# Optimization experiments

Measured on AMD Instinct MI355X. Metric: run time of the kernel, lower is better.

Reference implementation:

```python
import jax, jax.numpy as jnp
import numpy as np
import math

TWO_PI = 2.0 * math.pi
LN_EPS = 1e-5


def _phase(pos_f, d):
    # periods[i, j] = i * d + j + 2 ; phi[s, i, j] = cos(2*pi*k_s / periods[i, j])
    i = jnp.arange(d, dtype=jnp.float32)
    periods = i[:, None] * d + i[None, :] + 2.0  # (d, d)
    return jnp.cos(TWO_PI * pos_f[:, None, None] / periods)  # (S, d, d)


def _layernorm(x, g, b):
    mu = jnp.mean(x, axis=-1, keepdims=True)
    var = jnp.mean(jnp.square(x - mu), axis=-1, keepdims=True)
    return (x - mu) * jax.lax.rsqrt(var + LN_EPS) * g + b


def _pos_nk(x, P, phi):
    # Nk[b, s, i] = sum_j P[i, j] * x[b, s, j] * phi[s, i, j]
    return jnp.einsum('bsj,ij,sij->bsi', x, P, phi)


def setup_inputs() -> dict:
    key = jax.random.key(0)
    ks = jax.random.split(key, 10)
    B, S, V, D = 4, 4096, 64, 128
    NTOK = 64  # 4^3 k-mer tokens
    u = lambda k, shp, a: jax.random.uniform(k, shp, jnp.float32, -a, a)
    return {
        'tokens': jax.random.randint(ks[0], (B, S), 0, NTOK, dtype=jnp.int32),
        'positions': jnp.arange(S, dtype=jnp.int32),
        'emb': jax.random.normal(ks[1], (NTOK, V), jnp.float32),
        'char_P': u(ks[2], (V, V), 0.1),
        'M1': u(ks[3], (D, V), 0.5),
        'P1': u(ks[4], (D, D), 0.1),
        'g1': jnp.ones((D,), jnp.float32),
        'b1': jnp.zeros((D,), jnp.float32),
        'R1': u(ks[5], (D, V), 0.1),
        'M2': u(ks[6], (D, D), 0.5),
        'P2': u(ks[7], (D, D), 0.1),
        'g2': jnp.ones((D,), jnp.float32),
        'b2': jnp.zeros((D,), jnp.float32),
    }


def reference(tokens, positions, emb, char_P, M1, P1, g1, b1, R1, M2, P2, g2, b2):
    pos_f = positions.astype(jnp.float32)
    V, D1, D2 = emb.shape[1], M1.shape[0], M2.shape[0]
    # char level (Layer 0): embedding + position-modulated mixing
    x = emb[tokens]                               # (B, S, V)
    h = _pos_nk(x, char_P, _phase(pos_f, V))      # (B, S, V)
    # Layer 1: separate residual (in_dim != out_dim -> linear proj)
    t1 = jnp.einsum('bsj,ij->bsi', h, M1)         # (B, S, D1)
    n1 = _pos_nk(_layernorm(t1, g1, b1), P1, _phase(pos_f, D1))
    h1 = n1 + jnp.einsum('bsj,ij->bsi', h, R1)
    # Layer 2: shared residual (residual = x @ M.T, pre-norm)
    t2 = jnp.einsum('bsj,ij->bsi', h1, M2)        # (B, S, D2)
    n2 = _pos_nk(_layernorm(t2, g2, b2), P2, _phase(pos_f, D2))
    return n2 + t2
```

## Files before the change

kernel.cpp:

```cpp
#include <hip/hip_runtime.h>

typedef unsigned short u16;
typedef unsigned int   u32;
typedef float f32x2 __attribute__((ext_vector_type(2)));

#define BB 4
#define SS 4096
#define VV 64
#define DD 128

#define CPT_OFF 0
#define M1T_OFF 4096
#define R1T_OFF 12288
#define P1T_OFF 20480
#define M2T_OFF 36864
#define P2T_OFF 53248
#define EMB_OFF 69632
#define G1_OFF  73728
#define B1_OFF  73856
#define G2_OFF  73984
#define B2_OFF  74112
#define WS_F32_WEIGHTS 74240

__device__ __forceinline__ float bf2f(u16 u) {
    return __uint_as_float(((u32)u) << 16);
}
__device__ __forceinline__ float ldany(const void* p, int idx, bool f32) {
    return f32 ? ((const float*)p)[idx] : bf2f(((const u16*)p)[idx]);
}
__device__ __forceinline__ float phase_cos(float pos, float pf) {
    float x = pos * __builtin_amdgcn_rcpf(pf);
    float r = __builtin_amdgcn_fractf(x);
    return __builtin_amdgcn_cosf(r);
}
__device__ __forceinline__ float f4get(float4 v, int i) {
    return i == 0 ? v.x : i == 1 ? v.y : i == 2 ? v.z : v.w;
}
struct acc2x2 {
    f32x2 lo, hi;
    __device__ __forceinline__ void zero() { lo = (f32x2)0.f; hi = (f32x2)0.f; }
    __device__ __forceinline__ void fma(float s, float4 v) {
        f32x2 s2 = {s, s};
        f32x2 vlo = {v.x, v.y}, vhi = {v.z, v.w};
        lo = __builtin_elementwise_fma(s2, vlo, lo);
        hi = __builtin_elementwise_fma(s2, vhi, hi);
    }
    __device__ __forceinline__ float get(int b) const {
        return b == 0 ? lo[0] : b == 1 ? lo[1] : b == 2 ? hi[0] : hi[1];
    }
    __device__ __forceinline__ void red_xor(int m) {
        lo[0] += __shfl_xor(lo[0], m, 64);
        lo[1] += __shfl_xor(lo[1], m, 64);
        hi[0] += __shfl_xor(hi[0], m, 64);
        hi[1] += __shfl_xor(hi[1], m, 64);
    }
};

__global__ void prep_ws(const void* __restrict__ cP,  const void* __restrict__ M1,
                        const void* __restrict__ R1,  const void* __restrict__ P1,
                        const void* __restrict__ M2,  const void* __restrict__ P2,
                        const void* __restrict__ emb, const void* __restrict__ g1,
                        const void* __restrict__ b1,  const void* __restrict__ g2,
                        const void* __restrict__ b2,  float* __restrict__ wsf)
{
    const bool f32 = (((const u32*)g1)[0] == 0x3F800000u);
    const int m = blockIdx.x;
    const int t = threadIdx.x;
    if (m == 17) {
        for (int idx = t; idx < 4608; idx += 256) {
            float v; int dst;
            if (idx < 4096) { v = ldany(emb, idx, f32); dst = EMB_OFF + idx; }
            else {
                int off = idx - 4096, which = off >> 7, e = off & 127;
                const void* p = (which == 0) ? g1 : (which == 1) ? b1
                              : (which == 2) ? g2 : b2;
                v = ldany(p, e, f32);
                dst = G1_OFF + which * 128 + e;
            }
            wsf[dst] = v;
        }
        return;
    }
    __shared__ float tile[64][65];
    const void* src; int doff, R, C, ti0, tj0;
    if (m == 0)      { src = cP; doff = CPT_OFF; R = 64;  C = 64;  ti0 = 0;            tj0 = 0; }
    else if (m <= 2) { src = M1; doff = M1T_OFF; R = 128; C = 64;  ti0 = (m - 1) * 64; tj0 = 0; }
    else if (m <= 4) { src = R1; doff = R1T_OFF; R = 128; C = 64;  ti0 = (m - 3) * 64; tj0 = 0; }
    else {
        const int k = m - 5, w = k >> 2, q = k & 3;
        src  = (w == 0) ? P1 : (w == 1) ? M2 : P2;
        doff = (w == 0) ? P1T_OFF : (w == 1) ? M2T_OFF : P2T_OFF;
        R = 128; C = 128; ti0 = (q >> 1) * 64; tj0 = (q & 1) * 64;
    }
    float* dst = wsf + doff;
    #pragma unroll
    for (int k = 0; k < 16; ++k) {
        int idx = k * 256 + t;
        int i = idx >> 6, j = idx & 63;
        tile[i][j] = ldany(src, (ti0 + i) * C + (tj0 + j), f32);
    }
    __syncthreads();
    #pragma unroll
    for (int k = 0; k < 16; ++k) {
        int idx = k * 256 + t;
        int j = idx >> 6, i = idx & 63;
        int gj = tj0 + j, gi = ti0 + i;
        dst[((gj >> 2) * R + gi) * 4 + (gj & 3)] = tile[i][j];
    }
}

template<bool WS>
__global__ void __launch_bounds__(256, 4)
fused_hier(const int* __restrict__ tokens,
           const int* __restrict__ positions,
           const void* __restrict__ emb,
           const void* __restrict__ cP,
           const void* __restrict__ M1,
           const void* __restrict__ P1,
           const void* __restrict__ g1,
           const void* __restrict__ b1,
           const void* __restrict__ R1,
           const void* __restrict__ M2,
           const void* __restrict__ P2,
           const void* __restrict__ g2,
           const void* __restrict__ b2,
           const float* __restrict__ wsf,
           float* __restrict__ out)
{
    __shared__ float4 x4v[VV];
    __shared__ float4 h4v[VV];
    __shared__ float4 lnv[DD];
    __shared__ float4 h1v[DD];
    __shared__ float  t14p[4 * DD];
    __shared__ float  t2p[4 * DD];

    float* x4  = (float*)x4v;
    float* h4  = (float*)h4v;
    float* lnf = (float*)lnv;
    float* h1f = (float*)h1v;

    const int t = threadIdx.x;
    const int s = blockIdx.x;
    if (s >= SS) return;
    const bool f32 = WS ? true : (((const u32*)g1)[0] == 0x3F800000u);
    const float pos = (float)positions[s];
    const int wv = t >> 6, L = t & 63;
    const int i7 = wv * 32 + (L & 31);
    const int jh = L >> 5;
    const int i6 = wv * 16 + (L & 15);
    const int jq = (L >> 4) & 3;
    const int w  = wv, l = L;

    {
        int tok = tokens[wv * SS + s];
        int ie  = t & 63;
        float v = WS ? wsf[EMB_OFF + tok * VV + ie] : ldany(emb, tok * VV + ie, f32);
        x4[ie * 4 + wv] = v;
    }
    __syncthreads();

    {
        acc2x2 a; a.zero();
        const int jb = jq * 16;
        float pf = (float)(i6 * VV + jb + 2);
        #pragma unroll
        for (int q = 0; q < 4; ++q) {
            const int jg = jq * 4 + q;
            float4 w4;
            if (WS) w4 = *(const float4*)&wsf[CPT_OFF + (jg * VV + i6) * 4];
            #pragma unroll
            for (int k = 0; k < 4; ++k) {
                const int j = jb + q * 4 + k;
                float c  = phase_cos(pos, pf);
                float wt = (WS ? f4get(w4, k) : ldany(cP, i6 * VV + j, f32)) * c;
                a.fma(wt, x4v[j]);
                pf += 1.0f;
            }
        }
        a.red_xor(16);
        a.red_xor(32);
        h4[i6 * 4 + jq] = a.get(jq);
    }
    __syncthreads();

    float resv0, resv1;
    {
        acc2x2 at, ar; at.zero(); ar.zero();
        #pragma unroll
        for (int q = 0; q < 8; ++q) {
            const int jg = jh * 8 + q;
            float4 m4, r4;
            if (WS) {
                m4 = *(const float4*)&wsf[M1T_OFF + (jg * DD + i7) * 4];
                r4 = *(const float4*)&wsf[R1T_OFF + (jg * DD + i7) * 4];
            }
            #pragma unroll
            for (int k = 0; k < 4; ++k) {
                const int j = jh * 32 + q * 4 + k;
                float mv = WS ? f4get(m4, k) : ldany(M1, i7 * VV + j, f32);
                float rv = WS ? f4get(r4, k) : ldany(R1, i7 * VV + j, f32);
                float4 hb = h4v[j];
                at.fma(mv, hb);
                ar.fma(rv, hb);
            }
        }
        at.red_xor(32);
        ar.red_xor(32);
        const int b0 = jh * 2, b1 = b0 + 1;
        t14p[b0 * 128 + i7] = at.get(b0);
        t14p[b1 * 128 + i7] = at.get(b1);
        resv0 = ar.get(b0);
        resv1 = ar.get(b1);
    }
    __syncthreads();

    {
        float v0 = t14p[w * 128 + l], v1 = t14p[w * 128 + 64 + l];
        float s1 = v0 + v1;
        #pragma unroll
        for (int m = 1; m < 64; m <<= 1) s1 += __shfl_xor(s1, m, 64);
        float mu = s1 * (1.0f / 128.0f);
        float d0 = v0 - mu, d1 = v1 - mu;
        float s2 = d0 * d0 + d1 * d1;
        #pragma unroll
        for (int m = 1; m < 64; m <<= 1) s2 += __shfl_xor(s2, m, 64);
        float rs = rsqrtf(s2 * (1.0f / 128.0f) + 1e-5f);
        float ga = WS ? wsf[G1_OFF + l]      : ldany(g1, l, f32);
        float gb = WS ? wsf[G1_OFF + l + 64] : ldany(g1, l + 64, f32);
        float ba = WS ? wsf[B1_OFF + l]      : ldany(b1, l, f32);
        float bb = WS ? wsf[B1_OFF + l + 64] : ldany(b1, l + 64, f32);
        lnf[l * 4 + w]        = d0 * rs * ga + ba;
        lnf[(l + 64) * 4 + w] = d1 * rs * gb + bb;
    }
    __syncthreads();

    {
        acc2x2 acc; acc.zero();
        float pf = (float)(i7 * DD + jh * 64 + 2);
        #pragma unroll
        for (int q = 0; q < 16; ++q) {
            const int jg = jh * 16 + q;
            float4 w4;
            if (WS) w4 = *(const float4*)&wsf[P1T_OFF + (jg * DD + i7) * 4];
            #pragma unroll
            for (int k = 0; k < 4; ++k) {
                const int j = jh * 64 + q * 4 + k;
                float c = phase_cos(pos, pf);
                float wt = (WS ? f4get(w4, k) : ldany(P1, i7 * DD + j, f32)) * c;
                acc.fma(wt, lnv[j]);
                pf += 1.0f;
            }
        }
        acc.red_xor(32);
        const int b0 = jh * 2, b1 = b0 + 1;
        h1f[i7 * 4 + b0] = resv0 + acc.get(b0);
        h1f[i7 * 4 + b1] = resv1 + acc.get(b1);
    }
    __syncthreads();

    float t2v0, t2v1;
    {
        acc2x2 acc; acc.zero();
        #pragma unroll
        for (int q = 0; q < 16; ++q) {
            const int jg = jh * 16 + q;
            float4 m4;
            if (WS) m4 = *(const float4*)&wsf[M2T_OFF + (jg * DD + i7) * 4];
            #pragma unroll
            for (int k = 0; k < 4; ++k) {
                const int j = jh * 64 + q * 4 + k;
                float mv = WS ? f4get(m4, k) : ldany(M2, i7 * DD + j, f32);
                acc.fma(mv, h1v[j]);
            }
        }
        acc.red_xor(32);
        const int b0 = jh * 2, b1 = b0 + 1;
        t2p[b0 * 128 + i7] = acc.get(b0);
        t2p[b1 * 128 + i7] = acc.get(b1);
        t2v0 = acc.get(b0);
        t2v1 = acc.get(b1);
    }
    __syncthreads();

    {
        float v0 = t2p[w * 128 + l], v1 = t2p[w * 128 + 64 + l];
        float s1 = v0 + v1;
        #pragma unroll
        for (int m = 1; m < 64; m <<= 1) s1 += __shfl_xor(s1, m, 64);
        float mu = s1 * (1.0f / 128.0f);
        float d0 = v0 - mu, d1 = v1 - mu;
        float s2 = d0 * d0 + d1 * d1;
        #pragma unroll
        for (int m = 1; m < 64; m <<= 1) s2 += __shfl_xor(s2, m, 64);
        float rs = rsqrtf(s2 * (1.0f / 128.0f) + 1e-5f);
        float ga = WS ? wsf[G2_OFF + l]      : ldany(g2, l, f32);
        float gb = WS ? wsf[G2_OFF + l + 64] : ldany(g2, l + 64, f32);
        float ba = WS ? wsf[B2_OFF + l]      : ldany(b2, l, f32);
        float bb = WS ? wsf[B2_OFF + l + 64] : ldany(b2, l + 64, f32);
        lnf[l * 4 + w]        = d0 * rs * ga + ba;
        lnf[(l + 64) * 4 + w] = d1 * rs * gb + bb;
    }
    __syncthreads();

    {
        acc2x2 acc; acc.zero();
        float pf = (float)(i7 * DD + jh * 64 + 2);
        #pragma unroll
        for (int q = 0; q < 16; ++q) {
            const int jg = jh * 16 + q;
            float4 w4;
            if (WS) w4 = *(const float4*)&wsf[P2T_OFF + (jg * DD + i7) * 4];
            #pragma unroll
            for (int k = 0; k < 4; ++k) {
                const int j = jh * 64 + q * 4 + k;
                float c = phase_cos(pos, pf);
                float wt = (WS ? f4get(w4, k) : ldany(P2, i7 * DD + j, f32)) * c;
                acc.fma(wt, lnv[j]);
                pf += 1.0f;
            }
        }
        acc.red_xor(32);
        const int b0 = jh * 2, b1 = b0 + 1;
        out[(b0 * SS + s) * DD + i7] = acc.get(b0) + t2v0;
        out[(b1 * SS + s) * DD + i7] = acc.get(b1) + t2v1;
    }
}

extern "C" void kernel_launch(void* const* d_in, const int* in_sizes, int n_in,
                              void* d_out, int out_size, void* d_ws, size_t ws_size,
                              hipStream_t stream)
{
    const int* tokens    = (const int*)d_in[0];
    const int* positions = (const int*)d_in[1];
    const void* emb = d_in[2];
    const void* cP  = d_in[3];
    const void* M1  = d_in[4];
    const void* P1  = d_in[5];
    const void* g1  = d_in[6];
    const void* b1  = d_in[7];
    const void* R1  = d_in[8];
    const void* M2  = d_in[9];
    const void* P2  = d_in[10];
    const void* g2  = d_in[11];
    const void* b2  = d_in[12];
    float* out = (float*)d_out;
    float* wsf = (float*)d_ws;

    const bool tw = (ws_size >= (size_t)WS_F32_WEIGHTS * sizeof(float));
    if (tw) {
        prep_ws<<<18, 256, 0, stream>>>(cP, M1, R1, P1, M2, P2, emb,
                                        g1, b1, g2, b2, wsf);
        fused_hier<true><<<SS, 256, 0, stream>>>(tokens, positions, emb, cP, M1, P1,
                                                 g1, b1, R1, M2, P2, g2, b2, wsf, out);
    } else {
        fused_hier<false><<<SS, 256, 0, stream>>>(tokens, positions, emb, cP, M1, P1,
                                                  g1, b1, R1, M2, P2, g2, b2, wsf, out);
    }
}
```

Measured before the change: 144.4 us.

## Remap D=128 matvec stages to quarter-split rows with padded LDS vectors

```diff
diff --git a/kernel.cpp b/kernel.cpp
--- a/kernel.cpp
+++ b/kernel.cpp
@@ -110,7 +110,7 @@
 }
 
 template<bool WS>
-__global__ void __launch_bounds__(256, 4)
+__global__ void __launch_bounds__(256, 3)
 fused_hier(const int* __restrict__ tokens,
            const int* __restrict__ positions,
            const void* __restrict__ emb,
@@ -127,12 +127,13 @@
            const float* __restrict__ wsf,
            float* __restrict__ out)
 {
-    __shared__ float4 x4v[VV];
+    __shared__ float4 x4v[67];
     __shared__ float4 h4v[VV];
-    __shared__ float4 lnv[DD];
-    __shared__ float4 h1v[DD];
+    __shared__ float4 lnv[131];
+    __shared__ float4 h1v[131];
     __shared__ float  t14p[4 * DD];
     __shared__ float  t2p[4 * DD];
+    __shared__ float  resp[4 * DD];
 
     float* x4  = (float*)x4v;
     float* h4  = (float*)h4v;
@@ -145,45 +146,44 @@
     const bool f32 = WS ? true : (((const u32*)g1)[0] == 0x3F800000u);
     const float pos = (float)positions[s];
     const int wv = t >> 6, L = t & 63;
+    const int rp = wv * 16 + (L & 15);
+    const int jq = (L >> 4) & 3;
     const int i7 = wv * 32 + (L & 31);
     const int jh = L >> 5;
-    const int i6 = wv * 16 + (L & 15);
-    const int jq = (L >> 4) & 3;
     const int w  = wv, l = L;
 
     {
         int tok = tokens[wv * SS + s];
         int ie  = t & 63;
         float v = WS ? wsf[EMB_OFF + tok * VV + ie] : ldany(emb, tok * VV + ie, f32);
-        x4[ie * 4 + wv] = v;
+        x4[(ie + (ie >> 4)) * 4 + wv] = v;
     }
     __syncthreads();
 
     {
         acc2x2 a; a.zero();
         const int jb = jq * 16;
-        float pf = (float)(i6 * VV + jb + 2);
+        float pf = (float)(rp * VV + jb + 2);
         #pragma unroll
         for (int q = 0; q < 4; ++q) {
             const int jg = jq * 4 + q;
             float4 w4;
-            if (WS) w4 = *(const float4*)&wsf[CPT_OFF + (jg * VV + i6) * 4];
+            if (WS) w4 = *(const float4*)&wsf[CPT_OFF + (jg * VV + rp) * 4];
             #pragma unroll
             for (int k = 0; k < 4; ++k) {
                 const int j = jb + q * 4 + k;
                 float c  = phase_cos(pos, pf);
-                float wt = (WS ? f4get(w4, k) : ldany(cP, i6 * VV + j, f32)) * c;
-                a.fma(wt, x4v[j]);
+                float wt = (WS ? f4get(w4, k) : ldany(cP, rp * VV + j, f32)) * c;
+                a.fma(wt, x4v[j + (j >> 4)]);
                 pf += 1.0f;
             }
         }
         a.red_xor(16);
         a.red_xor(32);
-        h4[i6 * 4 + jq] = a.get(jq);
-    }
-    __syncthreads();
-
-    float resv0, resv1;
+        h4[rp * 4 + jq] = a.get(jq);
+    }
+    __syncthreads();
+
     {
         acc2x2 at, ar; at.zero(); ar.zero();
         #pragma unroll
@@ -209,8 +209,8 @@
         const int b0 = jh * 2, b1 = b0 + 1;
         t14p[b0 * 128 + i7] = at.get(b0);
         t14p[b1 * 128 + i7] = at.get(b1);
-        resv0 = ar.get(b0);
-        resv1 = ar.get(b1);
+        resp[b0 * 128 + i7] = ar.get(b0);
+        resp[b1 * 128 + i7] = ar.get(b1);
     }
     __syncthreads();
 
@@ -229,56 +229,76 @@
         float gb = WS ? wsf[G1_OFF + l + 64] : ldany(g1, l + 64, f32);
         float ba = WS ? wsf[B1_OFF + l]      : ldany(b1, l, f32);
         float bb = WS ? wsf[B1_OFF + l + 64] : ldany(b1, l + 64, f32);
-        lnf[l * 4 + w]        = d0 * rs * ga + ba;
-        lnf[(l + 64) * 4 + w] = d1 * rs * gb + bb;
-    }
-    __syncthreads();
-
-    {
-        acc2x2 acc; acc.zero();
-        float pf = (float)(i7 * DD + jh * 64 + 2);
-        #pragma unroll
-        for (int q = 0; q < 16; ++q) {
-            const int jg = jh * 16 + q;
-            float4 w4;
-            if (WS) w4 = *(const float4*)&wsf[P1T_OFF + (jg * DD + i7) * 4];
-            #pragma unroll
-            for (int k = 0; k < 4; ++k) {
-                const int j = jh * 64 + q * 4 + k;
-                float c = phase_cos(pos, pf);
-                float wt = (WS ? f4get(w4, k) : ldany(P1, i7 * DD + j, f32)) * c;
-                acc.fma(wt, lnv[j]);
-                pf += 1.0f;
-            }
-        }
-        acc.red_xor(32);
-        const int b0 = jh * 2, b1 = b0 + 1;
-        h1f[i7 * 4 + b0] = resv0 + acc.get(b0);
-        h1f[i7 * 4 + b1] = resv1 + acc.get(b1);
+        const int pA = l + (l >> 5);
+        const int pB = l + 66 + (l >> 5);
+        lnf[pA * 4 + w] = d0 * rs * ga + ba;
+        lnf[pB * 4 + w] = d1 * rs * gb + bb;
+    }
+    __syncthreads();
+
+    {
+        acc2x2 alo, ahi; alo.zero(); ahi.zero();
+        const int jb = jq * 32;
+        float pfa = (float)(rp * DD + jb + 2);
+        float pfb = pfa + 8192.0f;
+        #pragma unroll
+        for (int q = 0; q < 8; ++q) {
+            const int jg = jq * 8 + q;
+            float4 wa, wb;
+            if (WS) {
+                wa = *(const float4*)&wsf[P1T_OFF + (jg * DD + rp) * 4];
+                wb = *(const float4*)&wsf[P1T_OFF + (jg * DD + rp + 64) * 4];
+            }
+            #pragma unroll
+            for (int k = 0; k < 4; ++k) {
+                const int j = jb + q * 4 + k;
+                float ca = phase_cos(pos, pfa);
+                float cb = phase_cos(pos, pfb);
+                float4 lnj = lnv[j + (j >> 5)];
+                float wva = WS ? f4get(wa, k) : ldany(P1, rp * DD + j, f32);
+                float wvb = WS ? f4get(wb, k) : ldany(P1, (rp + 64) * DD + j, f32);
+                alo.fma(wva * ca, lnj);
+                ahi.fma(wvb * cb, lnj);
+                pfa += 1.0f; pfb += 1.0f;
+            }
+        }
+        alo.red_xor(16); alo.red_xor(32);
+        ahi.red_xor(16); ahi.red_xor(32);
+        float r0 = resp[jq * 128 + rp];
+        float r1 = resp[jq * 128 + rp + 64];
+        h1f[(rp + (rp >> 5)) * 4 + jq]      = r0 + alo.get(jq);
+        h1f[(rp + 66 + (rp >> 5)) * 4 + jq] = r1 + ahi.get(jq);
     }
     __syncthreads();
 
     float t2v0, t2v1;
     {
-        acc2x2 acc; acc.zero();
-        #pragma unroll
-        for (int q = 0; q < 16; ++q) {
-            const int jg = jh * 16 + q;
-            float4 m4;
-            if (WS) m4 = *(const float4*)&wsf[M2T_OFF + (jg * DD + i7) * 4];
-            #pragma unroll
-            for (int k = 0; k < 4; ++k) {
-                const int j = jh * 64 + q * 4 + k;
-                float mv = WS ? f4get(m4, k) : ldany(M2, i7 * DD + j, f32);
-                acc.fma(mv, h1v[j]);
-            }
-        }
-        acc.red_xor(32);
-        const int b0 = jh * 2, b1 = b0 + 1;
-        t2p[b0 * 128 + i7] = acc.get(b0);
-        t2p[b1 * 128 + i7] = acc.get(b1);
-        t2v0 = acc.get(b0);
-        t2v1 = acc.get(b1);
+        acc2x2 alo, ahi; alo.zero(); ahi.zero();
+        const int jb = jq * 32;
+        #pragma unroll
+        for (int q = 0; q < 8; ++q) {
+            const int jg = jq * 8 + q;
+            float4 wa, wb;
+            if (WS) {
+                wa = *(const float4*)&wsf[M2T_OFF + (jg * DD + rp) * 4];
+                wb = *(const float4*)&wsf[M2T_OFF + (jg * DD + rp + 64) * 4];
+            }
+            #pragma unroll
+            for (int k = 0; k < 4; ++k) {
+                const int j = jb + q * 4 + k;
+                float4 hj = h1v[j + (j >> 5)];
+                float wva = WS ? f4get(wa, k) : ldany(M2, rp * DD + j, f32);
+                float wvb = WS ? f4get(wb, k) : ldany(M2, (rp + 64) * DD + j, f32);
+                alo.fma(wva, hj);
+                ahi.fma(wvb, hj);
+            }
+        }
+        alo.red_xor(16); alo.red_xor(32);
+        ahi.red_xor(16); ahi.red_xor(32);
+        t2v0 = alo.get(jq);
+        t2v1 = ahi.get(jq);
+        t2p[jq * 128 + rp]      = t2v0;
+        t2p[jq * 128 + rp + 64] = t2v1;
     }
     __syncthreads();
 
@@ -297,32 +317,43 @@
         float gb = WS ? wsf[G2_OFF + l + 64] : ldany(g2, l + 64, f32);
         float ba = WS ? wsf[B2_OFF + l]      : ldany(b2, l, f32);
         float bb = WS ? wsf[B2_OFF + l + 64] : ldany(b2, l + 64, f32);
-        lnf[l * 4 + w]        = d0 * rs * ga + ba;
-        lnf[(l + 64) * 4 + w] = d1 * rs * gb + bb;
-    }
-    __syncthreads();
-
-    {
-        acc2x2 acc; acc.zero();
-        float pf = (float)(i7 * DD + jh * 64 + 2);
-        #pragma unroll
-        for (int q = 0; q < 16; ++q) {
-            const int jg = jh * 16 + q;
-            float4 w4;
-            if (WS) w4 = *(const float4*)&wsf[P2T_OFF + (jg * DD + i7) * 4];
-            #pragma unroll
-            for (int k = 0; k < 4; ++k) {
-                const int j = jh * 64 + q * 4 + k;
-                float c = phase_cos(pos, pf);
-                float wt = (WS ? f4get(w4, k) : ldany(P2, i7 * DD + j, f32)) * c;
-                acc.fma(wt, lnv[j]);
-                pf += 1.0f;
-            }
-        }
-        acc.red_xor(32);
-        const int b0 = jh * 2, b1 = b0 + 1;
-        out[(b0 * SS + s) * DD + i7] = acc.get(b0) + t2v0;
-        out[(b1 * SS + s) * DD + i7] = acc.get(b1) + t2v1;
+        const int pA = l + (l >> 5);
+        const int pB = l + 66 + (l >> 5);
+        lnf[pA * 4 + w] = d0 * rs * ga + ba;
+        lnf[pB * 4 + w] = d1 * rs * gb + bb;
+    }
+    __syncthreads();
+
+    {
+        acc2x2 alo, ahi; alo.zero(); ahi.zero();
+        const int jb = jq * 32;
+        float pfa = (float)(rp * DD + jb + 2);
+        float pfb = pfa + 8192.0f;
+        #pragma unroll
+        for (int q = 0; q < 8; ++q) {
+            const int jg = jq * 8 + q;
+            float4 wa, wb;
+            if (WS) {
+                wa = *(const float4*)&wsf[P2T_OFF + (jg * DD + rp) * 4];
+                wb = *(const float4*)&wsf[P2T_OFF + (jg * DD + rp + 64) * 4];
+            }
+            #pragma unroll
+            for (int k = 0; k < 4; ++k) {
+                const int j = jb + q * 4 + k;
+                float ca = phase_cos(pos, pfa);
+                float cb = phase_cos(pos, pfb);
+                float4 lnj = lnv[j + (j >> 5)];
+                float wva = WS ? f4get(wa, k) : ldany(P2, rp * DD + j, f32);
+                float wvb = WS ? f4get(wb, k) : ldany(P2, (rp + 64) * DD + j, f32);
+                alo.fma(wva * ca, lnj);
+                ahi.fma(wvb * cb, lnj);
+                pfa += 1.0f; pfb += 1.0f;
+            }
+        }
+        alo.red_xor(16); alo.red_xor(32);
+        ahi.red_xor(16); ahi.red_xor(32);
+        out[(jq * SS + s) * DD + rp]      = alo.get(jq) + t2v0;
+        out[(jq * SS + s) * DD + rp + 64] = ahi.get(jq) + t2v1;
     }
 }
 
```

New measurement: 154.7 us. 1.07x slower.
